# Kernel optimization log

Measured on AMD Instinct MI355X. Metric: run time of the kernel, lower is better.

Reference implementation:

```python
import jax, jax.numpy as jnp
import numpy as np
from jax import lax

B, N = 8, 4096
NPOINT, RADIUS, NSAMPLE = 1024, 0.2, 32
MLP = [64, 64, 128]
FEAT = 64
ALPHA = 0.2          # LeakyReLU slope
BN_EPS = 1e-5        # BatchNorm eps (eval mode, running_mean=0, running_var=1)
BIG = 1e10


def setup_inputs() -> dict:
    key = jax.random.key(0)
    ks = jax.random.split(key, 16)
    xyz = jax.random.uniform(ks[0], (B, N, 3), dtype=jnp.float32)
    feats = jax.random.normal(ks[1], (B, N, FEAT), dtype=jnp.float32)
    d = {"points": jnp.concatenate([xyz, feats], axis=-1)}
    ch = [FEAT] + MLP
    for i in range(len(MLP)):
        d[f"W{i}"] = jax.random.normal(ks[2 + 3 * i], (ch[i + 1], ch[i]), dtype=jnp.float32) * 0.1
        d[f"b{i}"] = jnp.zeros((ch[i + 1],), jnp.float32)
        d[f"g{i}"] = jnp.ones((ch[i + 1],), jnp.float32)
        d[f"be{i}"] = jnp.zeros((ch[i + 1],), jnp.float32)
    d["a_att"] = jax.random.uniform(ks[12], (3 + MLP[-1], MLP[-1]), jnp.float32, -0.3, 0.3)
    return d


def _gather(points, idx):
    # points: [B, N, D], idx: [B, ...] -> [B, ..., D]
    return jax.vmap(lambda p, i: p[i])(points, idx)


def farthest_point_sample(xyz, npoint):
    # xyz: [B, N, 3] -> [B, npoint] (deterministic start at index 0)
    b, n, _ = xyz.shape
    def step(carry, _):
        distance, farthest = carry
        centered = jnp.take_along_axis(xyz, farthest[:, None, None], axis=1)  # [B,1,3]
        dist = jnp.sum((xyz - centered) ** 2, axis=-1)                        # [B,N]
        distance = jnp.minimum(distance, dist)
        return (distance, jnp.argmax(distance, axis=-1)), farthest
    init = (jnp.full((b, n), BIG, dtype=xyz.dtype), jnp.zeros((b,), dtype=jnp.int32))
    _, idxs = lax.scan(step, init, None, length=npoint)
    return jnp.transpose(idxs)  # [B, npoint]


def query_ball_point(nsample, radius, xyz, centered_xyz):
    # squared distances [B, npoint, N]
    d = (-2.0 * jnp.einsum('bpc,bnc->bpn', centered_xyz, xyz)
         + jnp.sum(centered_xyz ** 2, -1)[..., None]
         + jnp.sum(xyz ** 2, -1)[:, None, :])
    d = jnp.where(d > radius ** 2, BIG, d)
    order = jnp.argsort(d, axis=-1)[..., :nsample]                    # [B,np,ns]
    sv = jnp.take_along_axis(d, order, axis=-1)                       # sorted values
    first = order[..., 0:1]
    return jnp.where(sv == BIG, first, order)


def _mlp(x, params):
    # x: [..., C]; 1x1 conv + BN(eval, mean=0, var=1) + relu per layer
    for (W, b, g, be) in params:
        x = jnp.einsum('...c,oc->...o', x, W) + b
        x = x * (g / jnp.sqrt(1.0 + BN_EPS)) + be
        x = jax.nn.relu(x)
    return x


def reference(points, W0, b0, g0, be0, W1, b1, g1, be1, W2, b2, g2, be2, a_att):
    xyz = points[..., :3]
    feats = points[..., 3:]
    cidx = farthest_point_sample(xyz, NPOINT)          # [B, npoint]
    cxyz = _gather(xyz, cidx)                          # [B, npoint, 3]
    cfeat = _gather(feats, cidx)                       # [B, npoint, D]
    gidx = query_ball_point(NSAMPLE, RADIUS, xyz, cxyz)  # [B, npoint, nsample]
    gxyz = _gather(xyz, gidx)                          # [B, npoint, ns, 3]
    gfeat = _gather(feats, gidx)                       # [B, npoint, ns, D]

    params = [(W0, b0, g0, be0), (W1, b1, g1, be1), (W2, b2, g2, be2)]
    cfeat = _mlp(cfeat, params)                        # [B, npoint, D']
    gfeat = _mlp(gfeat, params)                        # [B, npoint, ns, D']

    cpts = jnp.concatenate([cxyz, cfeat], axis=-1)     # [B, npoint, 3+D']
    gpts = jnp.concatenate([gxyz, gfeat], axis=-1)     # [B, npoint, ns, 3+D']

    delta = gpts - cpts[:, :, None, :]
    att = jax.nn.leaky_relu(jnp.einsum('bpnc,cd->bpnd', delta, a_att), ALPHA)
    att = jax.nn.softmax(att, axis=2)                  # over nsample (eval: no dropout)
    gac = jnp.sum(att * gfeat, axis=2)                 # [B, npoint, D']
    return jnp.concatenate([cxyz, gac], axis=-1)       # [B, npoint, 3+D']
```

## Files before the change

kernel.cpp:

```cpp
#include <hip/hip_runtime.h>
#include <math.h>

#define NBATCH 8
#define NPTS 4096
#define NPOINT 1024
#define NSAMPLE 32
#define PTDIM 67
#define BIGF 1e10f

#define DPP_QUAD_XOR1 0xB1
#define DPP_QUAD_XOR2 0x4E
#define DPP_ROW_HALF_MIRROR 0x141
#define DPP_ROW_MIRROR 0x140
#define DPP_ROW_BCAST15 0x142
#define DPP_ROW_BCAST31 0x143

template <int CTRL>
__device__ inline float dpp_mov_f(float v) {
  int i = __float_as_int(v);
  return __int_as_float(__builtin_amdgcn_update_dpp(i, i, CTRL, 0xf, 0xf, false));
}
template <int CTRL>
__device__ inline unsigned dpp_mov_u(unsigned v) {
  return (unsigned)__builtin_amdgcn_update_dpp((int)v, (int)v, CTRL, 0xf, 0xf, false);
}
template <int CTRL>
__device__ inline void dpp_min2(unsigned& hi, unsigned& lo) {
  unsigned nh = dpp_mov_u<CTRL>(hi);
  unsigned nl = dpp_mov_u<CTRL>(lo);
  bool take = (nh < hi) || (nh == hi && nl < lo);
  hi = take ? nh : hi;
  lo = take ? nl : lo;
}
__device__ inline unsigned fmap(float d) {
  unsigned b = __float_as_uint(d);
  return ((int)b < 0) ? ~b : (b | 0x80000000u);
}
#define FMAP_INF 0xFF800000u

struct FpsS {
  unsigned long long slots[2][4];
  int cidxS[NPOINT];
  float4 C[NPTS];
};
struct MlpS {
  float w0[64 * 64], w1[64 * 64], w2[128 * 64];
  float bb0[64], ss0[64], ee0[64];
  float bb1[64], ss1[64], ee1[64];
  float bb2[128], ss2[128], ee2[128];
};
#define F1_SMEM (sizeof(MlpS) > sizeof(FpsS) ? sizeof(MlpS) : sizeof(FpsS))

__device__ void fps_body(char* smemRaw, const float* __restrict__ pts,
                         int* __restrict__ cidx, float* __restrict__ X,
                         float* __restrict__ Y, float* __restrict__ Z) {
  FpsS* S = (FpsS*)smemRaw;
  const int b = blockIdx.x, tid = threadIdx.x;
  const int w = tid >> 6, lane = tid & 63;
  const float* pb = pts + (size_t)b * NPTS * PTDIM;
  float px[16], py[16], pz[16], dl[16];
  #pragma unroll
  for (int k = 0; k < 16; k++) {
    int j = tid + (k << 8);
    const float* pj = pb + (size_t)j * PTDIM;
    float x = pj[0], y = pj[1], z = pj[2];
    px[k] = x; py[k] = y; pz[k] = z;
    S->C[j] = make_float4(x, y, z, 0.0f);
    X[b * NPTS + j] = x; Y[b * NPTS + j] = y; Z[b * NPTS + j] = z;
    dl[k] = BIGF;
  }
  __syncthreads();
  int f = 0;
  float4 c0 = S->C[0];
  float cx = c0.x, cy = c0.y, cz = c0.z;
  for (int t = 0; t < NPOINT; t++) {
    if (tid == 0) S->cidxS[t] = f;
    float bv = -1.0f; int bi = 0;
    #pragma unroll
    for (int k = 0; k < 16; k++) {
      float dx = __fsub_rn(px[k], cx);
      float dy = __fsub_rn(py[k], cy);
      float dz = __fsub_rn(pz[k], cz);
      float d = __fadd_rn(__fadd_rn(__fmul_rn(dx, dx), __fmul_rn(dy, dy)), __fmul_rn(dz, dz));
      float nd = fminf(dl[k], d);
      dl[k] = nd;
      if (nd > bv) { bv = nd; bi = tid + (k << 8); }
    }
    float m = bv;
    m = fmaxf(m, dpp_mov_f<DPP_QUAD_XOR1>(m));
    m = fmaxf(m, dpp_mov_f<DPP_QUAD_XOR2>(m));
    m = fmaxf(m, dpp_mov_f<DPP_ROW_HALF_MIRROR>(m));
    m = fmaxf(m, dpp_mov_f<DPP_ROW_MIRROR>(m));
    m = fmaxf(m, dpp_mov_f<DPP_ROW_BCAST15>(m));
    m = fmaxf(m, dpp_mov_f<DPP_ROW_BCAST31>(m));
    unsigned wmaxbits = (unsigned)__builtin_amdgcn_readlane(__float_as_int(m), 63);
    unsigned cand = (__float_as_uint(bv) == wmaxbits) ? (unsigned)bi : 0xFFFFFFFFu;
    cand = min(cand, dpp_mov_u<DPP_QUAD_XOR1>(cand));
    cand = min(cand, dpp_mov_u<DPP_QUAD_XOR2>(cand));
    cand = min(cand, dpp_mov_u<DPP_ROW_HALF_MIRROR>(cand));
    cand = min(cand, dpp_mov_u<DPP_ROW_MIRROR>(cand));
    cand = min(cand, dpp_mov_u<DPP_ROW_BCAST15>(cand));
    cand = min(cand, dpp_mov_u<DPP_ROW_BCAST31>(cand));
    unsigned jmin = (unsigned)__builtin_amdgcn_readlane((int)cand, 63);
    if (lane == 0)
      S->slots[t & 1][w] = ((unsigned long long)wmaxbits << 32) |
                           (unsigned long long)(NPTS - 1 - jmin);
    __syncthreads();
    unsigned long long s0 = S->slots[t & 1][0], s1 = S->slots[t & 1][1];
    unsigned long long s2 = S->slots[t & 1][2], s3 = S->slots[t & 1][3];
    unsigned long long m0 = s0 > s1 ? s0 : s1;
    unsigned long long m1 = s2 > s3 ? s2 : s3;
    unsigned long long best = m0 > m1 ? m0 : m1;
    f = NPTS - 1 - (int)(best & 0xFFFFFFFFull);
    float4 cc = S->C[f];
    cx = cc.x; cy = cc.y; cz = cc.z;
  }
  __syncthreads();
  for (int i = tid; i < NPOINT; i += 256) cidx[b * NPOINT + i] = S->cidxS[i];
}

__device__ void mlp_body(char* smemRaw, const float* __restrict__ pts,
    const float* __restrict__ W0, const float* __restrict__ B0, const float* __restrict__ G0, const float* __restrict__ E0,
    const float* __restrict__ W1, const float* __restrict__ B1, const float* __restrict__ G1, const float* __restrict__ E1,
    const float* __restrict__ W2, const float* __restrict__ B2, const float* __restrict__ G2, const float* __restrict__ E2,
    float* __restrict__ mfeat) {
  MlpS* S = (MlpS*)smemRaw;
  const float INVS = 0.99999500003750f;
  const int t = threadIdx.x;
  for (int i = t; i < 4096; i += 256) { S->w0[i] = W0[i]; S->w1[i] = W1[i]; }
  for (int i = t; i < 8192; i += 256) { S->w2[i] = W2[i]; }
  if (t < 64) {
    S->bb0[t] = B0[t]; S->ss0[t] = G0[t] * INVS; S->ee0[t] = E0[t];
    S->bb1[t] = B1[t]; S->ss1[t] = G1[t] * INVS; S->ee1[t] = E1[t];
  }
  if (t < 128) { S->bb2[t] = B2[t]; S->ss2[t] = G2[t] * INVS; S->ee2[t] = E2[t]; }
  __syncthreads();

  const size_t r = (size_t)(blockIdx.x - 8) * 256 + t;
  const float* xr = pts + r * PTDIM + 3;
  float x[64];
  #pragma unroll
  for (int c = 0; c < 64; c++) x[c] = xr[c];

  float h1[64];
  #pragma unroll
  for (int o = 0; o < 64; o++) {
    float acc = S->bb0[o];
    #pragma unroll
    for (int c = 0; c < 64; c += 4) {
      float4 wv = *(const float4*)&S->w0[o * 64 + c];
      acc = fmaf(wv.x, x[c], acc);
      acc = fmaf(wv.y, x[c + 1], acc);
      acc = fmaf(wv.z, x[c + 2], acc);
      acc = fmaf(wv.w, x[c + 3], acc);
    }
    h1[o] = fmaxf(fmaf(acc, S->ss0[o], S->ee0[o]), 0.0f);
  }
  float h2[64];
  #pragma unroll
  for (int o = 0; o < 64; o++) {
    float acc = S->bb1[o];
    #pragma unroll
    for (int c = 0; c < 64; c += 4) {
      float4 wv = *(const float4*)&S->w1[o * 64 + c];
      acc = fmaf(wv.x, h1[c], acc);
      acc = fmaf(wv.y, h1[c + 1], acc);
      acc = fmaf(wv.z, h1[c + 2], acc);
      acc = fmaf(wv.w, h1[c + 3], acc);
    }
    h2[o] = fmaxf(fmaf(acc, S->ss1[o], S->ee1[o]), 0.0f);
  }
  float* orow = mfeat + r * 128;
  #pragma unroll
  for (int o = 0; o < 128; o += 4) {
    float a0 = S->bb2[o], a1 = S->bb2[o + 1], a2 = S->bb2[o + 2], a3 = S->bb2[o + 3];
    #pragma unroll
    for (int c = 0; c < 64; c += 4) {
      float4 wv0 = *(const float4*)&S->w2[(o    ) * 64 + c];
      float4 wv1 = *(const float4*)&S->w2[(o + 1) * 64 + c];
      float4 wv2 = *(const float4*)&S->w2[(o + 2) * 64 + c];
      float4 wv3 = *(const float4*)&S->w2[(o + 3) * 64 + c];
      a0 = fmaf(wv0.x, h2[c], a0); a0 = fmaf(wv0.y, h2[c+1], a0); a0 = fmaf(wv0.z, h2[c+2], a0); a0 = fmaf(wv0.w, h2[c+3], a0);
      a1 = fmaf(wv1.x, h2[c], a1); a1 = fmaf(wv1.y, h2[c+1], a1); a1 = fmaf(wv1.z, h2[c+2], a1); a1 = fmaf(wv1.w, h2[c+3], a1);
      a2 = fmaf(wv2.x, h2[c], a2); a2 = fmaf(wv2.y, h2[c+1], a2); a2 = fmaf(wv2.z, h2[c+2], a2); a2 = fmaf(wv2.w, h2[c+3], a2);
      a3 = fmaf(wv3.x, h2[c], a3); a3 = fmaf(wv3.y, h2[c+1], a3); a3 = fmaf(wv3.z, h2[c+2], a3); a3 = fmaf(wv3.w, h2[c+3], a3);
    }
    float4 ov;
    ov.x = fmaxf(fmaf(a0, S->ss2[o    ], S->ee2[o    ]), 0.0f);
    ov.y = fmaxf(fmaf(a1, S->ss2[o + 1], S->ee2[o + 1]), 0.0f);
    ov.z = fmaxf(fmaf(a2, S->ss2[o + 2], S->ee2[o + 2]), 0.0f);
    ov.w = fmaxf(fmaf(a3, S->ss2[o + 3], S->ee2[o + 3]), 0.0f);
    *(float4*)(orow + o) = ov;
  }
}

__global__ __launch_bounds__(256) void f1_kernel(const float* __restrict__ pts,
    const float* __restrict__ W0, const float* __restrict__ B0, const float* __restrict__ G0, const float* __restrict__ E0,
    const float* __restrict__ W1, const float* __restrict__ B1, const float* __restrict__ G1, const float* __restrict__ E1,
    const float* __restrict__ W2, const float* __restrict__ B2, const float* __restrict__ G2, const float* __restrict__ E2,
    float* __restrict__ mfeat, int* __restrict__ cidx,
    float* __restrict__ X, float* __restrict__ Y, float* __restrict__ Z) {
  __shared__ __align__(16) char smem[F1_SMEM];
  if (blockIdx.x < 8)
    fps_body(smem, pts, cidx, X, Y, Z);
  else
    mlp_body(smem, pts, W0, B0, G0, E0, W1, B1, G1, E1, W2, B2, G2, E2, mfeat);
}

__device__ void ballq_body(const float* __restrict__ X, const float* __restrict__ Y,
                           const float* __restrict__ Z, const int* __restrict__ cidx,
                           int* __restrict__ gidx,
                           float (*dbuf)[512], int (*ibuf)[512]) {
  const int t = threadIdx.x;
  const int w = t >> 6, lane = t & 63;
  const int pc = blockIdx.x * 4 + w;
  const int b = pc >> 10;
  const float* Xb = X + b * NPTS;
  const float* Yb = Y + b * NPTS;
  const float* Zb = Z + b * NPTS;
  const int cI = cidx[pc];
  const float cx = Xb[cI], cy = Yb[cI], cz = Zb[cI];
  const float sc = __fadd_rn(__fadd_rn(__fmul_rn(cx, cx), __fmul_rn(cy, cy)), __fmul_rn(cz, cz));
  const float R2 = 0.04f;
  int cnt = 0;
  for (int rr = 0; rr < 64; rr++) {
    int nI = rr * 64 + lane;
    float px = Xb[nI], py = Yb[nI], pz = Zb[nI];
    float dot = __fadd_rn(__fadd_rn(__fmul_rn(cx, px), __fmul_rn(cy, py)), __fmul_rn(cz, pz));
    float sx  = __fadd_rn(__fadd_rn(__fmul_rn(px, px), __fmul_rn(py, py)), __fmul_rn(pz, pz));
    float d   = __fadd_rn(__fadd_rn(__fmul_rn(-2.0f, dot), sc), sx);
    bool pred = !(d > R2);
    unsigned long long mask = __ballot(pred);
    if (pred) {
      int pos = cnt + (int)__popcll(mask & ((1ull << lane) - 1ull));
      if (pos < 512) { dbuf[w][pos] = d; ibuf[w][pos] = nI; }
    }
    cnt += (int)__popcll(mask);
  }
  const int K = cnt < 512 ? cnt : 512;
  unsigned long long kk[8];
  #pragma unroll
  for (int k = 0; k < 8; k++) {
    int pos = lane + 64 * k;
    if (pos < K)
      kk[k] = ((unsigned long long)fmap(dbuf[w][pos]) << 32) | (unsigned)ibuf[w][pos];
    else
      kk[k] = ((unsigned long long)FMAP_INF << 32) | 0x7fffffffu;
  }
  int first = 0;
  int* gout = gidx + pc * NSAMPLE;
  for (int it = 0; it < NSAMPLE; it++) {
    unsigned long long best = kk[0];
    #pragma unroll
    for (int k = 1; k < 8; k++) if (kk[k] < best) best = kk[k];
    unsigned hi = (unsigned)(best >> 32), lo = (unsigned)best;
    dpp_min2<DPP_QUAD_XOR1>(hi, lo);
    dpp_min2<DPP_QUAD_XOR2>(hi, lo);
    dpp_min2<DPP_ROW_HALF_MIRROR>(hi, lo);
    dpp_min2<DPP_ROW_MIRROR>(hi, lo);
    dpp_min2<DPP_ROW_BCAST15>(hi, lo);
    dpp_min2<DPP_ROW_BCAST31>(hi, lo);
    unsigned blo = (unsigned)__builtin_amdgcn_readlane((int)lo, 63);
    #pragma unroll
    for (int k = 0; k < 8; k++)
      if ((unsigned)kk[k] == blo)
        kk[k] = (kk[k] & 0xFFFFFFFFull) | ((unsigned long long)FMAP_INF << 32);
    if (it == 0) first = (int)blo;
    if (lane == 0) gout[it] = (it < K) ? (int)blo : first;
  }
}

__device__ void proj_body(const float* __restrict__ X, const float* __restrict__ Y,
                          const float* __restrict__ Z, const float* __restrict__ mfeat,
                          const float* __restrict__ Aatt, float* __restrict__ P,
                          float* As ) {
  const int t = threadIdx.x;
  const int pb = blockIdx.x - 2048;
  const int grp = pb & 3;
  const int tile = pb >> 2;
  for (int i = t; i < 131 * 32; i += 256) {
    int c = i >> 5, col = i & 31;
    As[i] = Aatt[c * 128 + grp * 32 + col];
  }
  __syncthreads();
  const int r0 = tile * 512 + t * 2;
  float acc0[32], acc1[32];
  {
    float x0 = X[r0], y0 = Y[r0], z0 = Z[r0];
    float x1 = X[r0 + 1], y1 = Y[r0 + 1], z1 = Z[r0 + 1];
    #pragma unroll
    for (int j = 0; j < 32; j += 4) {
      float4 a0 = *(const float4*)&As[0 * 32 + j];
      float4 a1 = *(const float4*)&As[1 * 32 + j];
      float4 a2 = *(const float4*)&As[2 * 32 + j];
      acc0[j]   = fmaf(z0, a2.x, fmaf(y0, a1.x, x0 * a0.x));
      acc0[j+1] = fmaf(z0, a2.y, fmaf(y0, a1.y, x0 * a0.y));
      acc0[j+2] = fmaf(z0, a2.z, fmaf(y0, a1.z, x0 * a0.z));
      acc0[j+3] = fmaf(z0, a2.w, fmaf(y0, a1.w, x0 * a0.w));
      acc1[j]   = fmaf(z1, a2.x, fmaf(y1, a1.x, x1 * a0.x));
      acc1[j+1] = fmaf(z1, a2.y, fmaf(y1, a1.y, x1 * a0.y));
      acc1[j+2] = fmaf(z1, a2.z, fmaf(y1, a1.z, x1 * a0.z));
      acc1[j+3] = fmaf(z1, a2.w, fmaf(y1, a1.w, x1 * a0.w));
    }
  }
  const float* m0 = mfeat + (size_t)r0 * 128;
  const float* m1 = m0 + 128;
  for (int c = 0; c < 128; c += 4) {
    float4 v0 = *(const float4*)(m0 + c);
    float4 v1 = *(const float4*)(m1 + c);
    #pragma unroll
    for (int u = 0; u < 4; u++) {
      const float* arow = &As[(3 + c + u) * 32];
      float s0 = u == 0 ? v0.x : u == 1 ? v0.y : u == 2 ? v0.z : v0.w;
      float s1 = u == 0 ? v1.x : u == 1 ? v1.y : u == 2 ? v1.z : v1.w;
      #pragma unroll
      for (int j = 0; j < 32; j += 4) {
        float4 a = *(const float4*)&arow[j];
        acc0[j]   = fmaf(s0, a.x, acc0[j]);
        acc0[j+1] = fmaf(s0, a.y, acc0[j+1]);
        acc0[j+2] = fmaf(s0, a.z, acc0[j+2]);
        acc0[j+3] = fmaf(s0, a.w, acc0[j+3]);
        acc1[j]   = fmaf(s1, a.x, acc1[j]);
        acc1[j+1] = fmaf(s1, a.y, acc1[j+1]);
        acc1[j+2] = fmaf(s1, a.z, acc1[j+2]);
        acc1[j+3] = fmaf(s1, a.w, acc1[j+3]);
      }
    }
  }
  float* p0 = P + (size_t)r0 * 128 + grp * 32;
  float* p1 = p0 + 128;
  #pragma unroll
  for (int j = 0; j < 32; j += 4) {
    *(float4*)(p0 + j) = make_float4(acc0[j], acc0[j+1], acc0[j+2], acc0[j+3]);
    *(float4*)(p1 + j) = make_float4(acc1[j], acc1[j+1], acc1[j+2], acc1[j+3]);
  }
}

__global__ __launch_bounds__(256) void f2_kernel(
    const float* __restrict__ X, const float* __restrict__ Y, const float* __restrict__ Z,
    const int* __restrict__ cidx, int* __restrict__ gidx,
    const float* __restrict__ mfeat, const float* __restrict__ Aatt,
    float* __restrict__ P) {
  __shared__ float dbuf[4][512];
  __shared__ int   ibuf[4][512];
  __shared__ float As[131 * 32];
  if (blockIdx.x < 2048)
    ballq_body(X, Y, Z, cidx, gidx, dbuf, ibuf);
  else
    proj_body(X, Y, Z, mfeat, Aatt, P, As);
}

__global__ __launch_bounds__(256) void attn_kernel(
    const float* __restrict__ X, const float* __restrict__ Y, const float* __restrict__ Z,
    const float* __restrict__ mfeat, const float* __restrict__ P,
    const int* __restrict__ cidx, const int* __restrict__ gidx,
    float* __restrict__ out) {
  const int pc = (blockIdx.x & 7) * 1024 + (blockIdx.x >> 3);
  const int b = pc >> 10;
  const int t = threadIdx.x;
  const int n = t & 31, q = t >> 5;
  const int cI = cidx[pc];
  const int g = gidx[pc * NSAMPLE + n];
  const float* Pg = P + ((size_t)b * NPTS + g) * 128 + q * 16;
  const float* Pc = P + ((size_t)b * NPTS + cI) * 128 + q * 16;
  const float* Gf = mfeat + ((size_t)b * NPTS + g) * 128 + q * 16;
  float a[16], gfv[16];
  #pragma unroll
  for (int k = 0; k < 4; k++) {
    float4 vg = *(const float4*)(Pg + 4 * k);
    float4 vc = *(const float4*)(Pc + 4 * k);
    float4 vf = *(const float4*)(Gf + 4 * k);
    a[4*k]   = vg.x - vc.x; a[4*k+1] = vg.y - vc.y;
    a[4*k+2] = vg.z - vc.z; a[4*k+3] = vg.w - vc.w;
    gfv[4*k] = vf.x; gfv[4*k+1] = vf.y; gfv[4*k+2] = vf.z; gfv[4*k+3] = vf.w;
  }
  #pragma unroll
  for (int j = 0; j < 16; j++) a[j] = a[j] >= 0.0f ? a[j] : 0.2f * a[j];
  float mx[16];
  #pragma unroll
  for (int j = 0; j < 16; j++) mx[j] = a[j];
  #pragma unroll
  for (int off = 16; off >= 1; off >>= 1)
    #pragma unroll
    for (int j = 0; j < 16; j++) mx[j] = fmaxf(mx[j], __shfl_xor(mx[j], off));
  float e[16], s[16];
  #pragma unroll
  for (int j = 0; j < 16; j++) { e[j] = expf(a[j] - mx[j]); s[j] = e[j]; }
  #pragma unroll
  for (int off = 16; off >= 1; off >>= 1)
    #pragma unroll
    for (int j = 0; j < 16; j++) s[j] += __shfl_xor(s[j], off);
  float gac[16];
  #pragma unroll
  for (int j = 0; j < 16; j++) gac[j] = (e[j] / s[j]) * gfv[j];
  #pragma unroll
  for (int off = 16; off >= 1; off >>= 1)
    #pragma unroll
    for (int j = 0; j < 16; j++) gac[j] += __shfl_xor(gac[j], off);
  if (n == 0) {
    float* orow = out + (size_t)pc * 131;
    #pragma unroll
    for (int j = 0; j < 16; j++) orow[3 + q * 16 + j] = gac[j];
    if (q == 0) {
      orow[0] = X[b * NPTS + cI]; orow[1] = Y[b * NPTS + cI]; orow[2] = Z[b * NPTS + cI];
    }
  }
}

extern "C" void kernel_launch(void* const* d_in, const int* in_sizes, int n_in,
                              void* d_out, int out_size, void* d_ws, size_t ws_size,
                              hipStream_t stream) {
  const float* points = (const float*)d_in[0];
  const float* W0 = (const float*)d_in[1];
  const float* B0 = (const float*)d_in[2];
  const float* G0 = (const float*)d_in[3];
  const float* E0 = (const float*)d_in[4];
  const float* W1 = (const float*)d_in[5];
  const float* B1 = (const float*)d_in[6];
  const float* G1 = (const float*)d_in[7];
  const float* E1 = (const float*)d_in[8];
  const float* W2 = (const float*)d_in[9];
  const float* B2 = (const float*)d_in[10];
  const float* G2 = (const float*)d_in[11];
  const float* E2 = (const float*)d_in[12];
  const float* Aatt = (const float*)d_in[13];
  float* out = (float*)d_out;

  float* mfeat = (float*)d_ws;
  float* Pw = mfeat + (size_t)NBATCH * NPTS * 128;
  float* Xw = Pw + (size_t)NBATCH * NPTS * 128;
  float* Yw = Xw + NBATCH * NPTS;
  float* Zw = Yw + NBATCH * NPTS;
  int* cidxw = (int*)(Zw + NBATCH * NPTS);
  int* gidxw = cidxw + NBATCH * NPOINT;

  f1_kernel<<<8 + NBATCH * NPTS / 256, 256, 0, stream>>>(points,
      W0, B0, G0, E0, W1, B1, G1, E1, W2, B2, G2, E2, mfeat, cidxw, Xw, Yw, Zw);
  f2_kernel<<<2048 + 256, 256, 0, stream>>>(Xw, Yw, Zw, cidxw, gidxw, mfeat, Aatt, Pw);
  attn_kernel<<<NBATCH * NPOINT, 256, 0, stream>>>(Xw, Yw, Zw, mfeat, Pw, cidxw, gidxw, out);
}
```

Before: 928.5 us.

## Tree-reduce FPS argmax, vectorize ball query loads, use DPP softmax reductions

The FPS loop now takes a tree max over the 16 per-thread distances and only afterwards resolves the argmax index. This shortens the serial compare-and-select chain inside the latency-bound 1024-step loop. The ball query reads xyz as float4 (four points per lane), which reorders the candidate indices it emits, and f2 shares one raw shared-memory buffer between its two roles. The attention softmax uses DPP-based 32-lane reductions and divides once after summing, but the final sum order differs slightly from the reference.

```diff
diff --git a/kernel.cpp b/kernel.cpp
--- a/kernel.cpp
+++ b/kernel.cpp
@@ -37,6 +37,23 @@
   return ((int)b < 0) ? ~b : (b | 0x80000000u);
 }
 #define FMAP_INF 0xFF800000u
+
+__device__ inline float red32_max(float v) {
+  v = fmaxf(v, dpp_mov_f<DPP_QUAD_XOR1>(v));
+  v = fmaxf(v, dpp_mov_f<DPP_QUAD_XOR2>(v));
+  v = fmaxf(v, dpp_mov_f<DPP_ROW_HALF_MIRROR>(v));
+  v = fmaxf(v, dpp_mov_f<DPP_ROW_MIRROR>(v));
+  v = fmaxf(v, __shfl_xor(v, 16));
+  return v;
+}
+__device__ inline float red32_sum(float v) {
+  v += dpp_mov_f<DPP_QUAD_XOR1>(v);
+  v += dpp_mov_f<DPP_QUAD_XOR2>(v);
+  v += dpp_mov_f<DPP_ROW_HALF_MIRROR>(v);
+  v += dpp_mov_f<DPP_ROW_MIRROR>(v);
+  v += __shfl_xor(v, 16);
+  return v;
+}
 
 struct FpsS {
   unsigned long long slots[2][4];
@@ -75,17 +92,21 @@
   float cx = c0.x, cy = c0.y, cz = c0.z;
   for (int t = 0; t < NPOINT; t++) {
     if (tid == 0) S->cidxS[t] = f;
-    float bv = -1.0f; int bi = 0;
     #pragma unroll
     for (int k = 0; k < 16; k++) {
       float dx = __fsub_rn(px[k], cx);
       float dy = __fsub_rn(py[k], cy);
       float dz = __fsub_rn(pz[k], cz);
       float d = __fadd_rn(__fadd_rn(__fmul_rn(dx, dx), __fmul_rn(dy, dy)), __fmul_rn(dz, dz));
-      float nd = fminf(dl[k], d);
-      dl[k] = nd;
-      if (nd > bv) { bv = nd; bi = tid + (k << 8); }
-    }
+      dl[k] = fminf(dl[k], d);
+    }
+    float u0 = fmaxf(dl[0], dl[1]),  u1 = fmaxf(dl[2], dl[3]);
+    float u2 = fmaxf(dl[4], dl[5]),  u3 = fmaxf(dl[6], dl[7]);
+    float u4 = fmaxf(dl[8], dl[9]),  u5 = fmaxf(dl[10], dl[11]);
+    float u6 = fmaxf(dl[12], dl[13]), u7 = fmaxf(dl[14], dl[15]);
+    float v0 = fmaxf(u0, u1), v1 = fmaxf(u2, u3);
+    float v2 = fmaxf(u4, u5), v3 = fmaxf(u6, u7);
+    float bv = fmaxf(fmaxf(v0, v1), fmaxf(v2, v3));
     float m = bv;
     m = fmaxf(m, dpp_mov_f<DPP_QUAD_XOR1>(m));
     m = fmaxf(m, dpp_mov_f<DPP_QUAD_XOR2>(m));
@@ -94,7 +115,16 @@
     m = fmaxf(m, dpp_mov_f<DPP_ROW_BCAST15>(m));
     m = fmaxf(m, dpp_mov_f<DPP_ROW_BCAST31>(m));
     unsigned wmaxbits = (unsigned)__builtin_amdgcn_readlane(__float_as_int(m), 63);
-    unsigned cand = (__float_as_uint(bv) == wmaxbits) ? (unsigned)bi : 0xFFFFFFFFu;
+    unsigned c_[16];
+    #pragma unroll
+    for (int k = 0; k < 16; k++)
+      c_[k] = (__float_as_uint(dl[k]) == wmaxbits) ? (unsigned)(tid + (k << 8)) : 0xFFFFFFFFu;
+    unsigned q0 = min(c_[0], c_[1]),  q1 = min(c_[2], c_[3]);
+    unsigned q2 = min(c_[4], c_[5]),  q3 = min(c_[6], c_[7]);
+    unsigned q4 = min(c_[8], c_[9]),  q5 = min(c_[10], c_[11]);
+    unsigned q6 = min(c_[12], c_[13]), q7 = min(c_[14], c_[15]);
+    unsigned r0 = min(q0, q1), r1 = min(q2, q3), r2 = min(q4, q5), r3 = min(q6, q7);
+    unsigned cand = min(min(r0, r1), min(r2, r3));
     cand = min(cand, dpp_mov_u<DPP_QUAD_XOR1>(cand));
     cand = min(cand, dpp_mov_u<DPP_QUAD_XOR2>(cand));
     cand = min(cand, dpp_mov_u<DPP_ROW_HALF_MIRROR>(cand));
@@ -207,10 +237,14 @@
     mlp_body(smem, pts, W0, B0, G0, E0, W1, B1, G1, E1, W2, B2, G2, E2, mfeat);
 }
 
-__device__ void ballq_body(const float* __restrict__ X, const float* __restrict__ Y,
+#define F2_SMEM 16768
+
+__device__ void ballq_body(char* smemRaw,
+                           const float* __restrict__ X, const float* __restrict__ Y,
                            const float* __restrict__ Z, const int* __restrict__ cidx,
-                           int* __restrict__ gidx,
-                           float (*dbuf)[512], int (*ibuf)[512]) {
+                           int* __restrict__ gidx) {
+  float (*dbuf)[512] = (float (*)[512])smemRaw;
+  int   (*ibuf)[512] = (int (*)[512])(smemRaw + 4 * 512 * 4);
   const int t = threadIdx.x;
   const int w = t >> 6, lane = t & 63;
   const int pc = blockIdx.x * 4 + w;
@@ -223,19 +257,27 @@
   const float sc = __fadd_rn(__fadd_rn(__fmul_rn(cx, cx), __fmul_rn(cy, cy)), __fmul_rn(cz, cz));
   const float R2 = 0.04f;
   int cnt = 0;
-  for (int rr = 0; rr < 64; rr++) {
-    int nI = rr * 64 + lane;
-    float px = Xb[nI], py = Yb[nI], pz = Zb[nI];
-    float dot = __fadd_rn(__fadd_rn(__fmul_rn(cx, px), __fmul_rn(cy, py)), __fmul_rn(cz, pz));
-    float sx  = __fadd_rn(__fadd_rn(__fmul_rn(px, px), __fmul_rn(py, py)), __fmul_rn(pz, pz));
-    float d   = __fadd_rn(__fadd_rn(__fmul_rn(-2.0f, dot), sc), sx);
-    bool pred = !(d > R2);
-    unsigned long long mask = __ballot(pred);
-    if (pred) {
-      int pos = cnt + (int)__popcll(mask & ((1ull << lane) - 1ull));
-      if (pos < 512) { dbuf[w][pos] = d; ibuf[w][pos] = nI; }
-    }
-    cnt += (int)__popcll(mask);
+  for (int rr = 0; rr < 16; rr++) {
+    const int base = rr * 256 + lane * 4;
+    float4 px4 = *(const float4*)(Xb + base);
+    float4 py4 = *(const float4*)(Yb + base);
+    float4 pz4 = *(const float4*)(Zb + base);
+    #pragma unroll
+    for (int e = 0; e < 4; e++) {
+      float px = e == 0 ? px4.x : e == 1 ? px4.y : e == 2 ? px4.z : px4.w;
+      float py = e == 0 ? py4.x : e == 1 ? py4.y : e == 2 ? py4.z : py4.w;
+      float pz = e == 0 ? pz4.x : e == 1 ? pz4.y : e == 2 ? pz4.z : pz4.w;
+      float dot = __fadd_rn(__fadd_rn(__fmul_rn(cx, px), __fmul_rn(cy, py)), __fmul_rn(cz, pz));
+      float sx  = __fadd_rn(__fadd_rn(__fmul_rn(px, px), __fmul_rn(py, py)), __fmul_rn(pz, pz));
+      float d   = __fadd_rn(__fadd_rn(__fmul_rn(-2.0f, dot), sc), sx);
+      bool pred = !(d > R2);
+      unsigned long long mask = __ballot(pred);
+      if (pred) {
+        int pos = cnt + (int)__popcll(mask & ((1ull << lane) - 1ull));
+        if (pos < 512) { dbuf[w][pos] = d; ibuf[w][pos] = base + e; }
+      }
+      cnt += (int)__popcll(mask);
+    }
   }
   const int K = cnt < 512 ? cnt : 512;
   unsigned long long kk[8];
@@ -270,10 +312,11 @@
   }
 }
 
-__device__ void proj_body(const float* __restrict__ X, const float* __restrict__ Y,
+__device__ void proj_body(char* smemRaw,
+                          const float* __restrict__ X, const float* __restrict__ Y,
                           const float* __restrict__ Z, const float* __restrict__ mfeat,
-                          const float* __restrict__ Aatt, float* __restrict__ P,
-                          float* As ) {
+                          const float* __restrict__ Aatt, float* __restrict__ P) {
+  float* As = (float*)smemRaw;
   const int t = threadIdx.x;
   const int pb = blockIdx.x - 2048;
   const int grp = pb & 3;
@@ -341,13 +384,11 @@
     const int* __restrict__ cidx, int* __restrict__ gidx,
     const float* __restrict__ mfeat, const float* __restrict__ Aatt,
     float* __restrict__ P) {
-  __shared__ float dbuf[4][512];
-  __shared__ int   ibuf[4][512];
-  __shared__ float As[131 * 32];
+  __shared__ __align__(16) char smem[F2_SMEM];
   if (blockIdx.x < 2048)
-    ballq_body(X, Y, Z, cidx, gidx, dbuf, ibuf);
+    ballq_body(smem, X, Y, Z, cidx, gidx);
   else
-    proj_body(X, Y, Z, mfeat, Aatt, P, As);
+    proj_body(smem, X, Y, Z, mfeat, Aatt, P);
 }
 
 __global__ __launch_bounds__(256) void attn_kernel(
@@ -376,31 +417,20 @@
   }
   #pragma unroll
   for (int j = 0; j < 16; j++) a[j] = a[j] >= 0.0f ? a[j] : 0.2f * a[j];
-  float mx[16];
-  #pragma unroll
-  for (int j = 0; j < 16; j++) mx[j] = a[j];
-  #pragma unroll
-  for (int off = 16; off >= 1; off >>= 1)
-    #pragma unroll
-    for (int j = 0; j < 16; j++) mx[j] = fmaxf(mx[j], __shfl_xor(mx[j], off));
-  float e[16], s[16];
-  #pragma unroll
-  for (int j = 0; j < 16; j++) { e[j] = expf(a[j] - mx[j]); s[j] = e[j]; }
-  #pragma unroll
-  for (int off = 16; off >= 1; off >>= 1)
-    #pragma unroll
-    for (int j = 0; j < 16; j++) s[j] += __shfl_xor(s[j], off);
-  float gac[16];
-  #pragma unroll
-  for (int j = 0; j < 16; j++) gac[j] = (e[j] / s[j]) * gfv[j];
-  #pragma unroll
-  for (int off = 16; off >= 1; off >>= 1)
-    #pragma unroll
-    for (int j = 0; j < 16; j++) gac[j] += __shfl_xor(gac[j], off);
+  float e[16], s[16], num[16];
+  #pragma unroll
+  for (int j = 0; j < 16; j++) {
+    float mx = red32_max(a[j]);
+    e[j] = expf(a[j] - mx);
+  }
+  #pragma unroll
+  for (int j = 0; j < 16; j++) s[j] = red32_sum(e[j]);
+  #pragma unroll
+  for (int j = 0; j < 16; j++) num[j] = red32_sum(e[j] * gfv[j]);
   if (n == 0) {
     float* orow = out + (size_t)pc * 131;
     #pragma unroll
-    for (int j = 0; j < 16; j++) orow[3 + q * 16 + j] = gac[j];
+    for (int j = 0; j < 16; j++) orow[3 + q * 16 + j] = num[j] / s[j];
     if (q == 0) {
       orow[0] = X[b * NPTS + cI]; orow[1] = Y[b * NPTS + cI]; orow[2] = Z[b * NPTS + cI];
     }
```

Measured after the change: 897.3 us. -3.4%, faster.
